# Optimization experiments

Hardware: AMD Instinct MI355X
Metric: run time of the kernel (lower is better)

The kernel has to match this reference:

```python
import jax, jax.numpy as jnp
import numpy as np

# FrictionConfig constants (chosen in init_kwargs)
K_STEPS = 4
ETA = 0.1
ETA_DECAY = 0.9
MU_MAX = 10.0
SMOOTH_LAMBDA = 0.1
RADIUS = 8
B, S, H = 4, 2048, 1024
INNER = max(H // 2, 32)  # 512


def _build_window_edges(length, radius):
    chunks = []
    for d in range(1, radius + 1):
        i = np.arange(length - d, dtype=np.int32)
        chunks.append(np.stack([i, i + d], axis=1))
    return np.concatenate(chunks, axis=0)  # [E, 2]


def setup_inputs() -> dict:
    key = jax.random.key(0)
    ks = jax.random.split(key, 8)
    hidden = jax.random.normal(ks[0], (B, S, H), dtype=jnp.float32)
    attention_mask = jnp.ones((B, S), dtype=jnp.int32)
    edges = jnp.asarray(_build_window_edges(S, RADIUS))
    # edge_mlp: Linear(2, INNER) -> GELU -> Linear(INNER, 1)
    W1 = jax.random.normal(ks[1], (2, INNER), dtype=jnp.float32) * (1.0 / np.sqrt(2))
    b1 = jnp.zeros((INNER,), dtype=jnp.float32)
    W2 = jax.random.normal(ks[2], (INNER, 1), dtype=jnp.float32) * (1.0 / np.sqrt(INNER))
    b2 = jnp.zeros((1,), dtype=jnp.float32)
    # q_proj: Linear(H, H)
    Wq = jax.random.normal(ks[3], (H, H), dtype=jnp.float32) * (1.0 / np.sqrt(H))
    bq = jnp.zeros((H,), dtype=jnp.float32)
    # LayerNorm
    gamma = jnp.ones((H,), dtype=jnp.float32)
    beta = jnp.zeros((H,), dtype=jnp.float32)
    return {"hidden": hidden, "attention_mask": attention_mask, "edges": edges,
            "Wq": Wq, "bq": bq, "W1": W1, "b1": b1, "W2": W2, "b2": b2,
            "gamma": gamma, "beta": beta}


def _edge_weights(h, ei, ej, W1, b1, W2, b2):
    hi = h[ei]  # [E, H]
    hj = h[ej]
    diff = hi - hj
    dist = jnp.linalg.norm(diff, axis=-1, keepdims=True)           # [E, 1]
    ni = jnp.maximum(jnp.linalg.norm(hi, axis=-1), 1e-6)
    nj = jnp.maximum(jnp.linalg.norm(hj, axis=-1), 1e-6)
    cos = (jnp.sum(hi * hj, axis=-1) / (ni * nj))[:, None]         # [E, 1]
    feats = jnp.concatenate([dist, cos], axis=-1)                  # [E, 2]
    z = jax.nn.gelu(feats @ W1 + b1, approximate=False) @ W2 + b2  # [E, 1]
    return jax.nn.softplus(z) + 1e-5


def _laplacian(h, ei, ej, mu):
    n = h.shape[0]
    weighted = mu * (h[ei] - h[ej])  # [E, H]
    # normalize_laplacian = True
    w = mu[:, 0]
    deg = jnp.zeros((n,), h.dtype).at[ei].add(w).at[ej].add(w)
    inv_sqrt = jnp.maximum(deg, 1e-6) ** -0.5
    weighted = weighted * (inv_sqrt[ei] * inv_sqrt[ej])[:, None]
    lap = jnp.zeros_like(h).at[ei].add(weighted).at[ej].add(-weighted)
    return lap


def _smooth(s):
    left = jnp.concatenate([s[:1], s[:-1]], axis=0)
    right = jnp.concatenate([s[1:], s[-1:]], axis=0)
    return s - SMOOTH_LAMBDA * (2.0 * s - left - right)


def _layernorm(x, gamma, beta):
    m = x.mean(axis=-1, keepdims=True)
    v = x.var(axis=-1, keepdims=True)
    return (x - m) * jax.lax.rsqrt(v + 1e-5) * gamma + beta


def _run_single(h, ei, ej, Wq, bq, W1, b1, W2, b2, gamma, beta):
    q = h @ Wq + bq
    state = h
    mu = None
    for step in range(K_STEPS):
        mu = _edge_weights(state, ei, ej, W1, b1, W2, b2)  # recompute_mu=True
        mu = jnp.minimum(mu, MU_MAX)
        lap = _laplacian(state, ei, ej, mu)
        eta = ETA * (ETA_DECAY ** step)
        state = state - eta * (lap - q)
        state = _smooth(state)
    out = _layernorm(state + h, gamma, beta)
    diffs = state[ei] - state[ej]
    energy = 0.5 * jnp.sum(mu[:, 0] * jnp.sum(diffs * diffs, axis=-1))
    return out, energy


def reference(hidden, attention_mask, edges, Wq, bq, W1, b1, W2, b2, gamma, beta):
    # All masks are full-length, so edges are identical across batch and
    # the outer Python batch loop vectorizes to a vmap.
    ei, ej = edges[:, 0], edges[:, 1]
    outputs, energy = jax.vmap(
        lambda h: _run_single(h, ei, ej, Wq, bq, W1, b1, W2, b2, gamma, beta)
    )(hidden)
    return outputs, energy
```

## Files before the change

kernel.cpp:

```cpp
#include <hip/hip_runtime.h>

#define BB 4
#define SS 2048
#define HH 1024
#define TQ 32
#define TU 32
#define CW 256

typedef unsigned short u16;
typedef __bf16 bf16x8 __attribute__((ext_vector_type(8)));
typedef float f32x4 __attribute__((ext_vector_type(4)));

__device__ __forceinline__ float b2f(u16 u){
  union { unsigned int i; float f; } v; v.i = ((unsigned int)u) << 16; return v.f;
}
__device__ __forceinline__ u16 f2b(float f){
  union { float f; unsigned int i; } v; v.f = f;
  unsigned int x = v.i;
  return (u16)((x + 0x7fffu + ((x >> 16) & 1u)) >> 16);
}
__device__ __forceinline__ float4 u4f(ushort4 v){
  float4 o; o.x = b2f(v.x); o.y = b2f(v.y); o.z = b2f(v.z); o.w = b2f(v.w); return o;
}
__device__ __forceinline__ ushort4 f4u(float4 v){
  ushort4 o; o.x = f2b(v.x); o.y = f2b(v.y); o.z = f2b(v.z); o.w = f2b(v.w); return o;
}
__device__ __forceinline__ float wave_sum(float v){
  #pragma unroll
  for(int m = 32; m > 0; m >>= 1) v += __shfl_xor(v, m);
  return v;
}
__device__ __forceinline__ float pread(const void* p, int i, int f){
  return f ? b2f(((const u16*)p)[i]) : ((const float*)p)[i];
}
__device__ __forceinline__ void gload16(const void* g, void* l){
  __builtin_amdgcn_global_load_lds((const __attribute__((address_space(1))) unsigned int*)g,
                                   (__attribute__((address_space(3))) unsigned int*)l, 16, 0, 0);
}
__device__ __forceinline__ float fast_gelu(float z){
  float x  = z * 0.70710678118654752f;
  float ax = fabsf(x);
  float t  = __builtin_amdgcn_rcpf(fmaf(0.3275911f, ax, 1.f));
  float poly = ((((1.061405429f*t - 1.453152027f)*t + 1.421413741f)*t
                 - 0.284496736f)*t + 0.254829592f)*t;
  float er = fmaf(-poly, __expf(-ax*ax), 1.f);
  er = (x < 0.f) ? -er : er;
  return 0.5f*z*(1.f + er);
}

__global__ __launch_bounds__(256) void k_params(const void* bq, const void* W1, const void* b1,
                                                const void* W2, const void* b2, const void* gm,
                                                const void* bt, float* bqc, float* W1c, float* b1c,
                                                float* W2c, float* b2c, float* gmc, float* btc,
                                                int* flagp){
  __shared__ int sf;
  if(threadIdx.x == 0){
    int f = (((const u16*)gm)[0] == 0x3F80u) ? 1 : 0;
    sf = f; *flagp = f;
  }
  __syncthreads();
  int f = sf, t = threadIdx.x;
  for(int i = t; i < 1024; i += 256) bqc[i] = pread(bq, i, f);
  for(int i = t; i < 1024; i += 256) W1c[i] = pread(W1, i, f);
  for(int i = t; i <  512; i += 256) b1c[i] = pread(b1, i, f);
  for(int i = t; i <  512; i += 256) W2c[i] = pread(W2, i, f);
  if(t == 0) b2c[0] = pread(b2, 0, f);
  for(int i = t; i < 1024; i += 256) gmc[i] = pread(gm, i, f);
  for(int i = t; i < 1024; i += 256) btc[i] = pread(bt, i, f);
}

__global__ __launch_bounds__(256) void k_cvt(const void* h, u16* s, const int* flagp){
  int f = *flagp;
  size_t i4 = (size_t)blockIdx.x*256 + threadIdx.x;
  if(f){
    ((ushort4*)s)[i4] = ((const ushort4*)h)[i4];
  } else {
    float4 v = ((const float4*)h)[i4];
    ((ushort4*)s)[i4] = f4u(v);
  }
}

__global__ __launch_bounds__(256) void k_transpose(const void* W, u16* __restrict__ Wt,
                                                   const int* flagp){
  int f = *flagp;
  __shared__ u16 t[32][33];
  int bx = blockIdx.x, by = blockIdx.y;
  int tx = threadIdx.x, ty = threadIdx.y;
  #pragma unroll
  for(int r = 0; r < 32; r += 8){
    int idx = (by*32 + ty + r)*HH + bx*32 + tx;
    float v = f ? b2f(((const u16*)W)[idx]) : ((const float*)W)[idx];
    t[ty + r][tx] = f2b(v);
  }
  __syncthreads();
  #pragma unroll
  for(int r = 0; r < 32; r += 8)
    Wt[(size_t)(bx*32 + ty + r)*HH + by*32 + tx] = t[tx][ty + r];
}

__global__ __launch_bounds__(256) void k_qgemm(const u16* __restrict__ A, const u16* __restrict__ Wt,
                                               const float* __restrict__ bqc, u16* __restrict__ q){
  __shared__ u16 lA[128*32];
  __shared__ u16 lB[128*32];
  int m0 = blockIdx.x*128, n0 = blockIdx.y*128;
  int tid  = threadIdx.x;
  int wave = tid >> 6, lane = tid & 63;
  int wm = (wave >> 1)*64, wn = (wave & 1)*64;
  int quad = lane >> 4, l16 = lane & 15;
  int srow = tid >> 2;
  int scol = (tid & 3)*8;

  f32x4 acc[4][4];
  #pragma unroll
  for(int i = 0; i < 4; i++)
    #pragma unroll
    for(int j = 0; j < 4; j++) acc[i][j] = (f32x4){0.f,0.f,0.f,0.f};

  for(int k0 = 0; k0 < HH; k0 += 32){
    __syncthreads();
    gload16(A  + (size_t)(m0 + srow     )*HH + k0 + scol, &lA[ srow     *32 + scol]);
    gload16(A  + (size_t)(m0 + srow + 64)*HH + k0 + scol, &lA[(srow+64) *32 + scol]);
    gload16(Wt + (size_t)(n0 + srow     )*HH + k0 + scol, &lB[ srow     *32 + scol]);
    gload16(Wt + (size_t)(n0 + srow + 64)*HH + k0 + scol, &lB[(srow+64) *32 + scol]);
    __syncthreads();
    bf16x8 af[4];
    #pragma unroll
    for(int mt = 0; mt < 4; mt++)
      af[mt] = *(const bf16x8*)&lA[(wm + mt*16 + l16)*32 + quad*8];
    #pragma unroll
    for(int nt = 0; nt < 4; nt++){
      bf16x8 bf = *(const bf16x8*)&lB[(wn + nt*16 + l16)*32 + quad*8];
      #pragma unroll
      for(int mt = 0; mt < 4; mt++)
        acc[mt][nt] = __builtin_amdgcn_mfma_f32_16x16x32_bf16(af[mt], bf, acc[mt][nt], 0, 0, 0);
    }
  }
  #pragma unroll
  for(int nt = 0; nt < 4; nt++){
    int col = n0 + wn + nt*16 + l16;
    float bqv = bqc[col];
    #pragma unroll
    for(int mt = 0; mt < 4; mt++){
      #pragma unroll
      for(int r = 0; r < 4; r++){
        int row = m0 + wm + mt*16 + quad*4 + r;
        q[(size_t)row*HH + col] = f2b(acc[mt][nt][r] + bqv);
      }
    }
  }
}

__global__ __launch_bounds__(512) void k_gram_mu(const u16* __restrict__ s,
                                                 const float* __restrict__ W1c, const float* __restrict__ b1c,
                                                 const float* __restrict__ W2c, const float* __restrict__ b2c,
                                                 float* __restrict__ mu){
  __shared__ float Gband[40*9];
  __shared__ float4 wpk[512];
  int b = blockIdx.y, i0 = blockIdx.x*TQ;
  int tid = threadIdx.x, wave = tid >> 6, lane = tid & 63;

  if(tid < 512) wpk[tid] = make_float4(W1c[tid], W1c[512+tid], b1c[tid], W2c[tid]);

  if(wave < 4){
    int ti = wave >> 1;
    int tj = (wave + 1) >> 1;
    int quad = lane >> 4, l16 = lane & 15;
    int ra = i0 + ti*16 + l16; if(ra > SS-1) ra = SS-1;
    int rb = i0 + tj*16 + l16; if(rb > SS-1) rb = SS-1;
    const u16* ar = s + ((size_t)b*SS + ra)*HH + quad*8;
    const u16* br = s + ((size_t)b*SS + rb)*HH + quad*8;
    f32x4 acc = (f32x4){0.f,0.f,0.f,0.f};
    #pragma unroll 8
    for(int k0 = 0; k0 < HH; k0 += 32){
      bf16x8 af = *(const bf16x8*)(ar + k0);
      bf16x8 bf = *(const bf16x8*)(br + k0);
      acc = __builtin_amdgcn_mfma_f32_16x16x32_bf16(af, bf, acc, 0, 0, 0);
    }
    #pragma unroll
    for(int r = 0; r < 4; r++){
      int gr = ti*16 + quad*4 + r;
      int dd = tj*16 + l16 - gr;
      if(dd >= 0 && dd <= 8) Gband[gr*9 + dd] = acc[r];
    }
  } else {
    for(int rr = wave - 4; rr < 8; rr += 4){
      int r = 32 + rr;
      int row = i0 + r; if(row > SS-1) row = SS-1;
      const ushort4* rp = (const ushort4*)(s + ((size_t)b*SS + row)*HH);
      float a = 0.f;
      #pragma unroll
      for(int c = 0; c < 4; c++){
        float4 v = u4f(rp[lane + 64*c]);
        a += v.x*v.x + v.y*v.y + v.z*v.z + v.w*v.w;
      }
      a = wave_sum(a);
      if(lane == 0) Gband[r*9] = a;
    }
  }
  __syncthreads();

  int e = tid >> 1, h = tid & 1;
  int d = (e >> 5) + 1, k = e & 31;
  bool valid = (i0 + k + d) < SS;
  float gii = Gband[k*9], gjj = Gband[(k+d)*9], gij = Gband[k*9 + d];
  float dist = sqrtf(fmaxf(gii + gjj - 2.f*gij, 0.f));
  float ni = fmaxf(sqrtf(gii), 1e-6f);
  float nj = fmaxf(sqrtf(gjj), 1e-6f);
  float cosv = gij * __builtin_amdgcn_rcpf(ni * nj);
  float acc = 0.f;
  const float4* wp = &wpk[h*256];
  #pragma unroll 4
  for(int j0 = 0; j0 < 256; j0++){
    float4 wv = wp[j0];
    float z1 = fmaf(dist, wv.x, fmaf(cosv, wv.y, wv.z));
    acc = fmaf(fast_gelu(z1), wv.w, acc);
  }
  acc += __shfl_xor(acc, 1);
  if(h == 0 && valid){
    float z  = acc + b2c[0];
    float sp = fmaxf(z, 0.f) + __logf(1.f + __expf(-fabsf(z)));
    mu[((size_t)b*8 + (d-1))*SS + (i0 + k)] = fminf(sp + 1e-5f, 10.0f);
  }
}

__global__ __launch_bounds__(256) void k_upsm(const u16* __restrict__ sIn, u16* __restrict__ sOut,
                                              const u16* __restrict__ q, const float* __restrict__ mu,
                                              float eta){
  __shared__ u16 st[50*CW];
  __shared__ u16 up[34*CW];
  __shared__ float invsS[50];
  __shared__ float muS[58*8];
  int i0 = blockIdx.x*TU, c0 = blockIdx.y*CW, b = blockIdx.z;
  int tid = threadIdx.x;

  for(int idx = tid; idx < 58*8; idx += 256){
    int ir = idx >> 3, d = (idx & 7) + 1;
    int i = i0 - 17 + ir;
    float v = 0.f;
    if(i >= 0 && i + d < SS) v = mu[((size_t)b*8 + d-1)*SS + i];
    muS[idx] = v;
  }
  for(int idx = tid; idx < 50*(CW/4); idx += 256){
    int r = idx / (CW/4), cc = idx % (CW/4);
    int i = i0 - 9 + r;
    ushort4 v = {0,0,0,0};
    if(i >= 0 && i < SS) v = *(const ushort4*)(sIn + ((size_t)b*SS + i)*HH + c0 + cc*4);
    ((ushort4*)st)[idx] = v;
  }
  __syncthreads();
  if(tid < 50){
    int ir = tid + 8;
    float deg = 0.f;
    #pragma unroll
    for(int d = 1; d <= 8; d++){
      deg += muS[ir*8 + d-1];
      deg += muS[(ir-d)*8 + d-1];
    }
    invsS[tid] = 1.0f / sqrtf(fmaxf(deg, 1e-6f));
  }
  __syncthreads();

  int rq = tid >> 6, lane = tid & 63;
  for(int jr = 0; jr < 9; jr++){
    int r = rq + jr*4;
    if(r >= 34) break;
    int i = i0 - 1 + r;
    if(i < 0 || i >= SS) continue;
    int sr = r + 8, vr = r + 8, mr = r + 16;
    float inv_i = invsS[vr];
    float4 si = u4f(((const ushort4*)(st + (size_t)sr*CW))[lane]);
    float A = 0.f;
    float4 acc = {0.f,0.f,0.f,0.f};
    #pragma unroll
    for(int d = 1; d <= 8; d++){
      float cR = muS[mr*8 + d-1]     * inv_i        * invsS[vr+d];
      float cL = muS[(mr-d)*8 + d-1] * invsS[vr-d]  * inv_i;
      A += cR + cL;
      float4 vR = u4f(((const ushort4*)(st + (size_t)(sr+d)*CW))[lane]);
      float4 vL = u4f(((const ushort4*)(st + (size_t)(sr-d)*CW))[lane]);
      acc.x -= cR*vR.x + cL*vL.x; acc.y -= cR*vR.y + cL*vL.y;
      acc.z -= cR*vR.z + cL*vL.z; acc.w -= cR*vR.w + cL*vL.w;
    }
    acc.x += A*si.x; acc.y += A*si.y; acc.z += A*si.z; acc.w += A*si.w;
    float4 qv = u4f(*(const ushort4*)(q + ((size_t)b*SS + i)*HH + c0 + lane*4));
    float4 o;
    o.x = si.x - eta*(acc.x - qv.x);
    o.y = si.y - eta*(acc.y - qv.y);
    o.z = si.z - eta*(acc.z - qv.z);
    o.w = si.w - eta*(acc.w - qv.w);
    ((ushort4*)(up + (size_t)r*CW))[lane] = f4u(o);
  }
  __syncthreads();
  for(int js = 0; js < 8; js++){
    int rr = rq + js*4;
    int i = i0 + rr;
    int ur = rr + 1;
    float4 c  = u4f(((const ushort4*)(up + (size_t)ur*CW))[lane]);
    float4 l  = (i > 0)      ? u4f(((const ushort4*)(up + (size_t)(ur-1)*CW))[lane]) : c;
    float4 r4 = (i < SS-1)   ? u4f(((const ushort4*)(up + (size_t)(ur+1)*CW))[lane]) : c;
    float4 o;
    o.x = c.x - 0.1f*(2.f*c.x - l.x - r4.x);
    o.y = c.y - 0.1f*(2.f*c.y - l.y - r4.y);
    o.z = c.z - 0.1f*(2.f*c.z - l.z - r4.z);
    o.w = c.w - 0.1f*(2.f*c.w - l.w - r4.w);
    *(ushort4*)(sOut + ((size_t)b*SS + i)*HH + c0 + lane*4) = f4u(o);
  }
}

__global__ __launch_bounds__(256) void k_out(const u16* __restrict__ sA, const void* __restrict__ hraw,
                                             const float* __restrict__ gmc, const float* __restrict__ btc,
                                             void* __restrict__ outp, const int* flagp){
  int f = *flagp;
  int b = blockIdx.x >> 11, i = blockIdx.x & (SS-1);
  int tid = threadIdx.x;
  size_t row = (size_t)b*SS + i;
  float4 sv = u4f(((const ushort4*)(sA + row*HH))[tid]);
  float4 hv;
  if(f) hv = u4f(((const ushort4*)((const u16*)hraw + row*HH))[tid]);
  else  hv = ((const float4*)((const float*)hraw + row*HH))[tid];
  float x0 = sv.x + hv.x, x1 = sv.y + hv.y, x2 = sv.z + hv.z, x3 = sv.w + hv.w;

  __shared__ float sh[4];
  int wv = tid >> 6, lane = tid & 63;
  float lsum = wave_sum(x0 + x1 + x2 + x3);
  if(lane == 0) sh[wv] = lsum;
  __syncthreads();
  float mean = (sh[0] + sh[1] + sh[2] + sh[3]) * (1.f/HH);
  __syncthreads();
  float d0 = x0-mean, d1 = x1-mean, d2 = x2-mean, d3 = x3-mean;
  float lsq = wave_sum(d0*d0 + d1*d1 + d2*d2 + d3*d3);
  if(lane == 0) sh[wv] = lsq;
  __syncthreads();
  float var = (sh[0] + sh[1] + sh[2] + sh[3]) * (1.f/HH);
  float sc = 1.0f / sqrtf(var + 1e-5f);

  int col = tid*4;
  float4 o;
  o.x = d0*sc*gmc[col+0] + btc[col+0];
  o.y = d1*sc*gmc[col+1] + btc[col+1];
  o.z = d2*sc*gmc[col+2] + btc[col+2];
  o.w = d3*sc*gmc[col+3] + btc[col+3];
  if(f) ((ushort4*)((u16*)outp + row*HH))[tid] = f4u(o);
  else  ((float4*)((float*)outp + row*HH))[tid] = o;
}

__global__ __launch_bounds__(512) void k_energy(const u16* __restrict__ s, const float* __restrict__ mu,
                                                float* __restrict__ partials){
  __shared__ float Gband[40*9];
  __shared__ float wacc[8];
  int b = blockIdx.y, i0 = blockIdx.x*TQ;
  int tid = threadIdx.x, wave = tid >> 6, lane = tid & 63;

  if(wave < 4){
    int ti = wave >> 1;
    int tj = (wave + 1) >> 1;
    int quad = lane >> 4, l16 = lane & 15;
    int ra = i0 + ti*16 + l16; if(ra > SS-1) ra = SS-1;
    int rb = i0 + tj*16 + l16; if(rb > SS-1) rb = SS-1;
    const u16* ar = s + ((size_t)b*SS + ra)*HH + quad*8;
    const u16* br = s + ((size_t)b*SS + rb)*HH + quad*8;
    f32x4 acc = (f32x4){0.f,0.f,0.f,0.f};
    #pragma unroll 8
    for(int k0 = 0; k0 < HH; k0 += 32){
      bf16x8 af = *(const bf16x8*)(ar + k0);
      bf16x8 bf = *(const bf16x8*)(br + k0);
      acc = __builtin_amdgcn_mfma_f32_16x16x32_bf16(af, bf, acc, 0, 0, 0);
    }
    #pragma unroll
    for(int r = 0; r < 4; r++){
      int gr = ti*16 + quad*4 + r;
      int dd = tj*16 + l16 - gr;
      if(dd >= 0 && dd <= 8) Gband[gr*9 + dd] = acc[r];
    }
  } else {
    for(int rr = wave - 4; rr < 8; rr += 4){
      int r = 32 + rr;
      int row = i0 + r; if(row > SS-1) row = SS-1;
      const ushort4* rp = (const ushort4*)(s + ((size_t)b*SS + row)*HH);
      float a = 0.f;
      #pragma unroll
      for(int c = 0; c < 4; c++){
        float4 v = u4f(rp[lane + 64*c]);
        a += v.x*v.x + v.y*v.y + v.z*v.z + v.w*v.w;
      }
      a = wave_sum(a);
      if(lane == 0) Gband[r*9] = a;
    }
  }
  __syncthreads();

  int d = wave + 1;
  int k = lane;
  float esum = 0.f;
  if(k < 32 && (i0 + k + d) < SS){
    float d2 = fmaxf(Gband[k*9] + Gband[(k+d)*9] - 2.f*Gband[k*9 + d], 0.f);
    esum = mu[((size_t)b*8 + (d-1))*SS + (i0 + k)] * d2;
  }
  esum = wave_sum(esum);
  if(lane == 0) wacc[wave] = esum;
  __syncthreads();
  if(tid == 0){
    float t = 0.f;
    #pragma unroll
    for(int w2 = 0; w2 < 8; w2++) t += wacc[w2];
    partials[(size_t)b*64 + blockIdx.x] = t;
  }
}

__global__ __launch_bounds__(64) void k_efinal(const float* __restrict__ partials, void* __restrict__ outp,
                                               const int* flagp){
  int f = *flagp;
  int b = blockIdx.x;
  float sacc = partials[(size_t)b*64 + threadIdx.x];
  sacc = wave_sum(sacc);
  if(threadIdx.x == 0){
    float e = 0.5f * sacc;
    if(f) ((u16*)outp)[(size_t)BB*SS*HH + b] = f2b(e);
    else  ((float*)outp)[(size_t)BB*SS*HH + b] = e;
  }
}

extern "C" void kernel_launch(void* const* d_in, const int* in_sizes, int n_in,
                              void* d_out, int out_size, void* d_ws, size_t ws_size,
                              hipStream_t stream) {
  const void* hidden = d_in[0];
  const void* Wq  = d_in[3];
  const void* bq  = d_in[4];
  const void* W1  = d_in[5];
  const void* b1  = d_in[6];
  const void* W2  = d_in[7];
  const void* b2v = d_in[8];
  const void* gamma = d_in[9];
  const void* beta  = d_in[10];

  char* w = (char*)d_ws;
  u16*   q   = (u16*)w;   w += (size_t)BB*SS*HH*2;
  u16*   sA  = (u16*)w;   w += (size_t)BB*SS*HH*2;
  u16*   Wt  = (u16*)w;   w += (size_t)HH*HH*2;
  float* mu  = (float*)w; w += (size_t)BB*8*SS*4;
  float* partials = (float*)w; w += (size_t)BB*64*4;
  float* bqc = (float*)w; w += 1024*4;
  float* W1c = (float*)w; w += 1024*4;
  float* b1c = (float*)w; w += 512*4;
  float* W2c = (float*)w; w += 512*4;
  float* b2c = (float*)w; w += 4;
  float* gmc = (float*)w; w += 1024*4;
  float* btc = (float*)w; w += 1024*4;
  int*   flagp = (int*)w; w += 4;
  u16* sB = (u16*)d_out;

  k_params   <<<1, 256, 0, stream>>>(bq, W1, b1, W2, b2v, gamma, beta,
                                     bqc, W1c, b1c, W2c, b2c, gmc, btc, flagp);
  k_cvt      <<<(BB*SS*HH/4)/256, 256, 0, stream>>>(hidden, sA, flagp);
  k_transpose<<<dim3(HH/32, HH/32), dim3(32,8), 0, stream>>>(Wq, Wt, flagp);
  k_qgemm    <<<dim3(BB*SS/128, HH/128), 256, 0, stream>>>(sA, Wt, bqc, q);

  const float etas[4] = {0.1f, 0.09f, 0.081f, 0.0729f};
  for(int step = 0; step < 4; step++){
    const u16* cur = (step & 1) ? sB : sA;
    u16*       nxt = (step & 1) ? sA : sB;
    k_gram_mu<<<dim3(SS/TQ, BB), 512, 0, stream>>>(cur, W1c, b1c, W2c, b2c, mu);
    k_upsm   <<<dim3(SS/TU, HH/CW, BB), 256, 0, stream>>>(cur, nxt, q, mu, etas[step]);
  }
  k_out   <<<BB*SS, 256, 0, stream>>>(sA, hidden, gmc, btc, d_out, flagp);
  k_energy<<<dim3(SS/TQ, BB), 512, 0, stream>>>(sA, mu, partials);
  k_efinal<<<BB, 64, 0, stream>>>(partials, d_out, flagp);
}
```

Measured before the change: 405.4 us.

## Shrink gram/mu tiles to 8 rows using single self-gram MFMA per block

The gram-band kernels now handle 8 query rows per block instead of 32. A single wave computes the 16x16 self-Gram of rows i0..i0+15 with one MFMA chain, replacing the four-wave cross-tile MFMAs and the separate norm waves. This launches four times as many smaller 128-thread blocks for better GPU occupancy and drops redundant tile loads. In exchange each row is reread by neighbouring blocks (16 rows loaded per 8 produced), and the energy partials and final reduction are resized to match.

Measured after the change: 415.8 us. +2.6%, slower.

```diff
diff --git a/kernel.cpp b/kernel.cpp
--- a/kernel.cpp
+++ b/kernel.cpp
@@ -3,7 +3,7 @@
 #define BB 4
 #define SS 2048
 #define HH 1024
-#define TQ 32
+#define TG 8
 #define TU 32
 #define CW 256
 
@@ -150,57 +150,40 @@
   }
 }
 
-__global__ __launch_bounds__(512) void k_gram_mu(const u16* __restrict__ s,
+__global__ __launch_bounds__(128) void k_gram_mu(const u16* __restrict__ s,
                                                  const float* __restrict__ W1c, const float* __restrict__ b1c,
                                                  const float* __restrict__ W2c, const float* __restrict__ b2c,
                                                  float* __restrict__ mu){
-  __shared__ float Gband[40*9];
+  __shared__ float Gband[16*9];
   __shared__ float4 wpk[512];
-  int b = blockIdx.y, i0 = blockIdx.x*TQ;
+  int b = blockIdx.y, i0 = blockIdx.x*TG;
   int tid = threadIdx.x, wave = tid >> 6, lane = tid & 63;
 
-  if(tid < 512) wpk[tid] = make_float4(W1c[tid], W1c[512+tid], b1c[tid], W2c[tid]);
-
-  if(wave < 4){
-    int ti = wave >> 1;
-    int tj = (wave + 1) >> 1;
+  #pragma unroll
+  for(int i = tid; i < 512; i += 128)
+    wpk[i] = make_float4(W1c[i], W1c[512+i], b1c[i], W2c[i]);
+
+  if(wave == 0){
     int quad = lane >> 4, l16 = lane & 15;
-    int ra = i0 + ti*16 + l16; if(ra > SS-1) ra = SS-1;
-    int rb = i0 + tj*16 + l16; if(rb > SS-1) rb = SS-1;
+    int ra = i0 + l16; if(ra > SS-1) ra = SS-1;
     const u16* ar = s + ((size_t)b*SS + ra)*HH + quad*8;
-    const u16* br = s + ((size_t)b*SS + rb)*HH + quad*8;
     f32x4 acc = (f32x4){0.f,0.f,0.f,0.f};
     #pragma unroll 8
     for(int k0 = 0; k0 < HH; k0 += 32){
       bf16x8 af = *(const bf16x8*)(ar + k0);
-      bf16x8 bf = *(const bf16x8*)(br + k0);
-      acc = __builtin_amdgcn_mfma_f32_16x16x32_bf16(af, bf, acc, 0, 0, 0);
+      acc = __builtin_amdgcn_mfma_f32_16x16x32_bf16(af, af, acc, 0, 0, 0);
     }
     #pragma unroll
     for(int r = 0; r < 4; r++){
-      int gr = ti*16 + quad*4 + r;
-      int dd = tj*16 + l16 - gr;
+      int gr = quad*4 + r;
+      int dd = l16 - gr;
       if(dd >= 0 && dd <= 8) Gband[gr*9 + dd] = acc[r];
     }
-  } else {
-    for(int rr = wave - 4; rr < 8; rr += 4){
-      int r = 32 + rr;
-      int row = i0 + r; if(row > SS-1) row = SS-1;
-      const ushort4* rp = (const ushort4*)(s + ((size_t)b*SS + row)*HH);
-      float a = 0.f;
-      #pragma unroll
-      for(int c = 0; c < 4; c++){
-        float4 v = u4f(rp[lane + 64*c]);
-        a += v.x*v.x + v.y*v.y + v.z*v.z + v.w*v.w;
-      }
-      a = wave_sum(a);
-      if(lane == 0) Gband[r*9] = a;
-    }
   }
   __syncthreads();
 
   int e = tid >> 1, h = tid & 1;
-  int d = (e >> 5) + 1, k = e & 31;
+  int d = (e >> 3) + 1, k = e & 7;
   bool valid = (i0 + k + d) < SS;
   float gii = Gband[k*9], gjj = Gband[(k+d)*9], gij = Gband[k*9 + d];
   float dist = sqrtf(fmaxf(gii + gjj - 2.f*gij, 0.f));
@@ -344,77 +327,53 @@
   else  ((float4*)((float*)outp + row*HH))[tid] = o;
 }
 
-__global__ __launch_bounds__(512) void k_energy(const u16* __restrict__ s, const float* __restrict__ mu,
+__global__ __launch_bounds__(128) void k_energy(const u16* __restrict__ s, const float* __restrict__ mu,
                                                 float* __restrict__ partials){
-  __shared__ float Gband[40*9];
-  __shared__ float wacc[8];
-  int b = blockIdx.y, i0 = blockIdx.x*TQ;
+  __shared__ float Gband[16*9];
+  int b = blockIdx.y, i0 = blockIdx.x*TG;
   int tid = threadIdx.x, wave = tid >> 6, lane = tid & 63;
 
-  if(wave < 4){
-    int ti = wave >> 1;
-    int tj = (wave + 1) >> 1;
+  if(wave == 0){
     int quad = lane >> 4, l16 = lane & 15;
-    int ra = i0 + ti*16 + l16; if(ra > SS-1) ra = SS-1;
-    int rb = i0 + tj*16 + l16; if(rb > SS-1) rb = SS-1;
+    int ra = i0 + l16; if(ra > SS-1) ra = SS-1;
     const u16* ar = s + ((size_t)b*SS + ra)*HH + quad*8;
-    const u16* br = s + ((size_t)b*SS + rb)*HH + quad*8;
     f32x4 acc = (f32x4){0.f,0.f,0.f,0.f};
     #pragma unroll 8
     for(int k0 = 0; k0 < HH; k0 += 32){
       bf16x8 af = *(const bf16x8*)(ar + k0);
-      bf16x8 bf = *(const bf16x8*)(br + k0);
-      acc = __builtin_amdgcn_mfma_f32_16x16x32_bf16(af, bf, acc, 0, 0, 0);
+      acc = __builtin_amdgcn_mfma_f32_16x16x32_bf16(af, af, acc, 0, 0, 0);
     }
     #pragma unroll
     for(int r = 0; r < 4; r++){
-      int gr = ti*16 + quad*4 + r;
-      int dd = tj*16 + l16 - gr;
+      int gr = quad*4 + r;
+      int dd = l16 - gr;
       if(dd >= 0 && dd <= 8) Gband[gr*9 + dd] = acc[r];
     }
-  } else {
-    for(int rr = wave - 4; rr < 8; rr += 4){
-      int r = 32 + rr;
-      int row = i0 + r; if(row > SS-1) row = SS-1;
-      const ushort4* rp = (const ushort4*)(s + ((size_t)b*SS + row)*HH);
-      float a = 0.f;
-      #pragma unroll
-      for(int c = 0; c < 4; c++){
-        float4 v = u4f(rp[lane + 64*c]);
-        a += v.x*v.x + v.y*v.y + v.z*v.z + v.w*v.w;
-      }
-      a = wave_sum(a);
-      if(lane == 0) Gband[r*9] = a;
-    }
-  }
-  __syncthreads();
-
-  int d = wave + 1;
-  int k = lane;
-  float esum = 0.f;
-  if(k < 32 && (i0 + k + d) < SS){
-    float d2 = fmaxf(Gband[k*9] + Gband[(k+d)*9] - 2.f*Gband[k*9 + d], 0.f);
-    esum = mu[((size_t)b*8 + (d-1))*SS + (i0 + k)] * d2;
-  }
-  esum = wave_sum(esum);
-  if(lane == 0) wacc[wave] = esum;
-  __syncthreads();
-  if(tid == 0){
-    float t = 0.f;
-    #pragma unroll
-    for(int w2 = 0; w2 < 8; w2++) t += wacc[w2];
-    partials[(size_t)b*64 + blockIdx.x] = t;
-  }
-}
-
-__global__ __launch_bounds__(64) void k_efinal(const float* __restrict__ partials, void* __restrict__ outp,
-                                               const int* flagp){
+  }
+  __syncthreads();
+  if(wave == 0){
+    int d = (lane >> 3) + 1, k = lane & 7;
+    float esum = 0.f;
+    if((i0 + k + d) < SS){
+      float d2 = fmaxf(Gband[k*9] + Gband[(k+d)*9] - 2.f*Gband[k*9 + d], 0.f);
+      esum = mu[((size_t)b*8 + (d-1))*SS + (i0 + k)] * d2;
+    }
+    esum = wave_sum(esum);
+    if(lane == 0) partials[(size_t)b*256 + blockIdx.x] = esum;
+  }
+}
+
+__global__ __launch_bounds__(256) void k_efinal(const float* __restrict__ partials, void* __restrict__ outp,
+                                                const int* flagp){
   int f = *flagp;
   int b = blockIdx.x;
-  float sacc = partials[(size_t)b*64 + threadIdx.x];
+  float sacc = partials[(size_t)b*256 + threadIdx.x];
   sacc = wave_sum(sacc);
+  __shared__ float sh[4];
+  if((threadIdx.x & 63) == 0) sh[threadIdx.x >> 6] = sacc;
+  __syncthreads();
   if(threadIdx.x == 0){
-    float e = 0.5f * sacc;
+    float e = 0.5f * (sh[0] + sh[1] + sh[2] + sh[3]);
     if(f) ((u16*)outp)[(size_t)BB*SS*HH + b] = f2b(e);
     else  ((float*)outp)[(size_t)BB*SS*HH + b] = e;
   }
@@ -438,7 +397,7 @@
   u16*   sA  = (u16*)w;   w += (size_t)BB*SS*HH*2;
   u16*   Wt  = (u16*)w;   w += (size_t)HH*HH*2;
   float* mu  = (float*)w; w += (size_t)BB*8*SS*4;
-  float* partials = (float*)w; w += (size_t)BB*64*4;
+  float* partials = (float*)w; w += (size_t)BB*256*4;
   float* bqc = (float*)w; w += 1024*4;
   float* W1c = (float*)w; w += 1024*4;
   float* b1c = (float*)w; w += 512*4;
@@ -459,10 +418,10 @@
   for(int step = 0; step < 4; step++){
     const u16* cur = (step & 1) ? sB : sA;
     u16*       nxt = (step & 1) ? sA : sB;
-    k_gram_mu<<<dim3(SS/TQ, BB), 512, 0, stream>>>(cur, W1c, b1c, W2c, b2c, mu);
+    k_gram_mu<<<dim3(SS/TG, BB), 128, 0, stream>>>(cur, W1c, b1c, W2c, b2c, mu);
     k_upsm   <<<dim3(SS/TU, HH/CW, BB), 256, 0, stream>>>(cur, nxt, q, mu, etas[step]);
   }
   k_out   <<<BB*SS, 256, 0, stream>>>(sA, hidden, gmc, btc, d_out, flagp);
-  k_energy<<<dim3(SS/TQ, BB), 512, 0, stream>>>(sA, mu, partials);
-  k_efinal<<<BB, 64, 0, stream>>>(partials, d_out, flagp);
-}
+  k_energy<<<dim3(SS/TG, BB), 128, 0, stream>>>(sA, mu, partials);
+  k_efinal<<<BB, 256, 0, stream>>>(partials, d_out, flagp);
+}
```
